# Kernel optimization log

Hardware: AMD Instinct MI355X
Metric: run time of the kernel (lower is better)

The kernel has to match this reference:

```python
import jax, jax.numpy as jnp
import numpy as np

N = 16000   # query points
M = 16000   # support points
NB = 32     # neighbors per query
A = 4       # kanchor (SO(2)/z-axis discrete anchors, kanchor<10 branch)
K = 15      # kernel points
CIN = 32
COUT = 32
RADIUS = 1.0
KP_EXTENT = 0.6


def _make_kernel_points(key):
    # KPConv-style kernel points inside a sphere of radius 0.66*RADIUS, first point at center
    kp = jax.random.normal(key, (K, 3), dtype=jnp.float32)
    kp = kp / (jnp.linalg.norm(kp, axis=-1, keepdims=True) + 1e-8)
    r = jax.random.uniform(jax.random.fold_in(key, 1), (K, 1), dtype=jnp.float32) ** (1.0 / 3.0)
    kp = kp * r * (0.66 * RADIUS)
    return kp.at[0].set(0.0)


def _make_anchors():
    # kanchor=4 -> rotations about z by 2*pi*a/A (E2PN get_anchors for kanchor<10)
    ang = 2.0 * jnp.pi * jnp.arange(A, dtype=jnp.float32) / A
    c, s = jnp.cos(ang), jnp.sin(ang)
    z = jnp.zeros_like(c)
    o = jnp.ones_like(c)
    return jnp.stack([c, -s, z, s, c, z, z, z, o], axis=-1).reshape(A, 3, 3)


def setup_inputs() -> dict:
    key = jax.random.key(0)
    k1, k2, k3, k4, k5, k6 = jax.random.split(key, 6)
    q_pts = jax.random.uniform(k1, (N, 3), dtype=jnp.float32) * 0.5
    s_pts = jax.random.uniform(k2, (M, 3), dtype=jnp.float32) * 0.5
    neighb_inds = jax.random.randint(k3, (N, NB), 0, M, dtype=jnp.int32)
    x = jax.random.normal(k4, (M, A, CIN), dtype=jnp.float32)
    kernel_points = _make_kernel_points(k5)
    anchors = _make_anchors()
    # kaiming-uniform-ish init of the (K, C_in, C_out) separable conv weights
    bound = float(np.sqrt(6.0 / ((1 + 5) * CIN)))
    weights = jax.random.uniform(k6, (K, CIN, COUT), dtype=jnp.float32,
                                 minval=-bound, maxval=bound)
    return {"q_pts": q_pts, "s_pts": s_pts, "neighb_inds": neighb_inds, "x": x,
            "kernel_points": kernel_points, "anchors": anchors, "weights": weights}


def reference(q_pts, s_pts, neighb_inds, x, kernel_points, anchors, weights):
    # neighbor gather, centered on query points: [N, NB, 3]
    neighbors = s_pts[neighb_inds] - q_pts[:, None, :]
    # rotate kernel points by each anchor: [A, K, 3]
    rot_kp = jnp.einsum('aij,kj->aki', anchors, kernel_points)
    # squared distances via |n|^2 + |kp|^2 - 2 n.kp (avoids [A,N,NB,K,3] blowup)
    n2 = jnp.sum(neighbors * neighbors, axis=-1)          # [N, NB]
    k2 = jnp.sum(rot_kp * rot_kp, axis=-1)                # [A, K]
    cross = jnp.einsum('nbj,akj->anbk', neighbors, rot_kp)
    sq_distances = n2[None, :, :, None] + k2[:, None, None, :] - 2.0 * cross  # [A,N,NB,K]
    # linear KP influence, clamped at 0
    all_weights = jnp.clip(1.0 - jnp.sqrt(jnp.maximum(sq_distances, 1e-12)) / KP_EXTENT,
                           0.0, None)                      # [A, N, NB, K]
    # gather neighbor features: [N, NB, A, C_in]
    neighb_x = x[neighb_inds]
    # weight neighbors onto kernel points (sum aggregation): [A, N, K, C_in]
    weighted_feats = jnp.einsum('anbk,nbac->ankc', all_weights, neighb_x)
    # per-kernel-point small GEMMs, summed over K: [N, A, C_out]
    out = jnp.einsum('ankc,kcd->nad', weighted_feats, weights)
    return out
```

## Files before the change

kernel.cpp:

```cpp
#include <hip/hip_runtime.h>


typedef short bf16x8 __attribute__((ext_vector_type(8)));
typedef float f32x4  __attribute__((ext_vector_type(4)));

__device__ __forceinline__ unsigned short f2bf(float f) {
    unsigned u = __builtin_bit_cast(unsigned, f);
    return (unsigned short)((u + 0x8000u) >> 16);
}

__device__ __forceinline__ unsigned pack2bf(float hi, float lo) {
    unsigned uh = __builtin_bit_cast(unsigned, hi) + 0x8000u;
    unsigned ul = __builtin_bit_cast(unsigned, lo) + 0x8000u;
    return __builtin_amdgcn_perm(uh, ul, 0x07060302u);
}

__global__ void prep_kernel(const float* __restrict__ W, unsigned short* __restrict__ Wp) {
    const int idx = blockIdx.x * 256 + threadIdx.x;
    const int kk = idx >> 10, d = (idx >> 5) & 31, e = idx & 31;
    const int kcs = kk * 32 + e;
    const int c = kcs >> 4, k = kcs & 15;
    const float v = (k < 15) ? W[(k * 32 + c) * 32 + d] : 0.0f;
    Wp[idx] = f2bf(v);
}

__global__ __launch_bounds__(256) void kpconv_mfma(
    const float* __restrict__ q_pts,
    const float* __restrict__ s_pts,
    const int*   __restrict__ inds,
    const float* __restrict__ x,
    const float* __restrict__ kp,
    const float* __restrict__ anchors,
    const unsigned short* __restrict__ Wp,
    float*       __restrict__ out)
{
    __shared__ __align__(16) unsigned short xa_s[16384];
    __shared__ __align__(16) unsigned short aw_s[8192];
    __shared__ __align__(16) float nbr[512];
    __shared__ __align__(16) float rk_s[256];
    __shared__ int sidx[128];

    const int t  = threadIdx.x;
    const int n0 = blockIdx.x * 4;

    if (t < 128) {
        const int q = t >> 5, b = t & 31;
        const int idx = inds[(n0 + q) * 32 + b];
        sidx[t] = idx;
        const float qx = q_pts[(n0 + q) * 3 + 0];
        const float qy = q_pts[(n0 + q) * 3 + 1];
        const float qz = q_pts[(n0 + q) * 3 + 2];
        const float nx = s_pts[idx * 3 + 0] - qx;
        const float ny = s_pts[idx * 3 + 1] - qy;
        const float nz = s_pts[idx * 3 + 2] - qz;
        float4 v; v.x = nx; v.y = ny; v.z = nz; v.w = nx*nx + ny*ny + nz*nz;
        *(float4*)&nbr[t * 4] = v;
    } else if (t < 192) {
        const int j = t - 128;
        const int a = j >> 4, k = j & 15;
        if (k < 15) {
            const float kx = kp[k*3+0], ky = kp[k*3+1], kz = kp[k*3+2];
            const float* R = anchors + a * 9;
            float4 v;
            v.x = R[0]*kx + R[1]*ky + R[2]*kz;
            v.y = R[3]*kx + R[4]*ky + R[5]*kz;
            v.z = R[6]*kx + R[7]*ky + R[8]*kz;
            v.w = v.x*v.x + v.y*v.y + v.z*v.z;
            *(float4*)&rk_s[(a * 16 + k) * 4] = v;
        }
    }
    __syncthreads();

    {
        const int c4 = t & 7, bg = (t >> 3) & 7, q = t >> 6;
        #pragma unroll
        for (int a = 0; a < 4; ++a) {
            float4 v[4];
            #pragma unroll
            for (int i = 0; i < 4; ++i) {
                const int row = sidx[q * 32 + 4 * bg + i];
                v[i] = ((const float4*)x)[row * 32 + a * 8 + c4];
            }
            const float* vp = (const float*)v;
            #pragma unroll
            for (int j = 0; j < 4; ++j) {
                const int c  = 4 * c4 + j;
                const int fc = c4 & 3;
                const int bb = 4 * (bg & 1) + 8 * ((bg >> 1) ^ fc);
                uint2 w;
                w.x = pack2bf(vp[1 * 4 + j], vp[0 * 4 + j]);
                w.y = pack2bf(vp[3 * 4 + j], vp[2 * 4 + j]);
                *(uint2*)&xa_s[((a * 4 + q) * 32 + c) * 32 + bb] = w;
            }
        }
    }

    {
        #pragma unroll
        for (int i = 0; i < 2; ++i) {
            const int tau = i * 256 + t;
            const int a = tau >> 7, q = (tau >> 5) & 3, b = tau & 31;
            const float4 nb = *(const float4*)&nbr[(q * 32 + b) * 4];
            unsigned short wv[16];
            #pragma unroll
            for (int k = 0; k < 15; ++k) {
                const float4 r = *(const float4*)&rk_s[(a * 16 + k) * 4];
                const float sq = nb.w + r.w - 2.0f * (nb.x*r.x + nb.y*r.y + nb.z*r.z);
                const float d = sqrtf(fmaxf(sq, 1e-12f));
                wv[k] = f2bf(fmaxf(1.0f - d * (1.0f / 0.6f), 0.0f));
            }
            wv[15] = 0;
            unsigned short* p = &aw_s[(a * 4 + q) * 512 + b];
            #pragma unroll
            for (int k = 0; k < 16; ++k) p[k * 32] = wv[k];
        }
    }
    __syncthreads();

    const int a    = t >> 6;
    const int lane = t & 63;
    const int l15  = lane & 15;
    const int quad = lane >> 4;

    unsigned short* wfb = &xa_s[a * 4096];

    #pragma unroll
    for (int q = 0; q < 4; ++q) {
        const bf16x8 afr = *(const bf16x8*)&aw_s[((a * 4 + q) * 16 + l15) * 32 + quad * 8];
        const int fc  = (l15 >> 2) & 3;
        const bf16x8 b0 = *(const bf16x8*)&xa_s[((a * 4 + q) * 32 + l15) * 32 + 8 * (quad ^ fc)];
        const bf16x8 b1 = *(const bf16x8*)&xa_s[((a * 4 + q) * 32 + l15 + 16) * 32 + 8 * (quad ^ fc)];
        f32x4 d0 = {0.f, 0.f, 0.f, 0.f}, d1 = {0.f, 0.f, 0.f, 0.f};
        d0 = __builtin_amdgcn_mfma_f32_16x16x32_bf16(afr, b0, d0, 0, 0, 0);
        d1 = __builtin_amdgcn_mfma_f32_16x16x32_bf16(afr, b1, d1, 0, 0, 0);
        uint2 s0, s1;
        s0.x = pack2bf(d0[1], d0[0]); s0.y = pack2bf(d0[3], d0[2]);
        s1.x = pack2bf(d1[1], d1[0]); s1.y = pack2bf(d1[3], d1[2]);
        *(uint2*)&wfb[q * 512 + l15 * 16 + quad * 4]        = s0;
        *(uint2*)&wfb[q * 512 + (l15 + 16) * 16 + quad * 4] = s1;
    }

    f32x4 o0 = {0.f, 0.f, 0.f, 0.f}, o1 = {0.f, 0.f, 0.f, 0.f};
    #pragma unroll
    for (int kk = 0; kk < 16; ++kk) {
        const bf16x8 a2 = *(const bf16x8*)&wfb[(l15 & 3) * 512 + kk * 32 + quad * 8];
        const bf16x8 w0 = *(const bf16x8*)&Wp[kk * 1024 + l15 * 32 + quad * 8];
        const bf16x8 w1 = *(const bf16x8*)&Wp[kk * 1024 + (l15 + 16) * 32 + quad * 8];
        o0 = __builtin_amdgcn_mfma_f32_16x16x32_bf16(a2, w0, o0, 0, 0, 0);
        o1 = __builtin_amdgcn_mfma_f32_16x16x32_bf16(a2, w1, o1, 0, 0, 0);
    }
    if (quad == 0) {
        #pragma unroll
        for (int r = 0; r < 4; ++r) {
            out[((n0 + r) * 4 + a) * 32 + l15]      = o0[r];
            out[((n0 + r) * 4 + a) * 32 + 16 + l15] = o1[r];
        }
    }
}

extern "C" void kernel_launch(void* const* d_in, const int* in_sizes, int n_in,
                              void* d_out, int out_size, void* d_ws, size_t ws_size,
                              hipStream_t stream) {
    const float* q_pts   = (const float*)d_in[0];
    const float* s_pts   = (const float*)d_in[1];
    const int*   inds    = (const int*)d_in[2];
    const float* x       = (const float*)d_in[3];
    const float* kp      = (const float*)d_in[4];
    const float* anchors = (const float*)d_in[5];
    const float* weights = (const float*)d_in[6];
    float*       out     = (float*)d_out;
    unsigned short* Wp   = (unsigned short*)d_ws;

    prep_kernel<<<dim3(64), dim3(256), 0, stream>>>(weights, Wp);
    kpconv_mfma<<<dim3(4000), dim3(256), 0, stream>>>(
        q_pts, s_pts, inds, x, kp, anchors, Wp, out);
}
```

Before: 126.7 us.

## Compute KP influence weights directly in MFMA A-fragment registers

Removes the aw_s shared buffer and its separate compute-and-scatter phase. Each lane now computes its 8 influence weights for the first MFMA's A fragment in registers, reading padded neighbor data (stride 36) and one rotated kernel point. The padded 16th kernel point gets a huge squared norm so its weight clamps to zero. The second-stage scratch writes and reads also get an XOR swizzle to reduce LDS bank conflicts. This cuts LDS traffic and footprint, which may raise occupancy, but the distance math is recomputed redundantly per lane.

```diff
diff --git a/kernel.cpp b/kernel.cpp
--- a/kernel.cpp
+++ b/kernel.cpp
@@ -35,8 +35,7 @@
     float*       __restrict__ out)
 {
     __shared__ __align__(16) unsigned short xa_s[16384];
-    __shared__ __align__(16) unsigned short aw_s[8192];
-    __shared__ __align__(16) float nbr[512];
+    __shared__ __align__(16) float nbr[576];
     __shared__ __align__(16) float rk_s[256];
     __shared__ int sidx[128];
 
@@ -54,20 +53,22 @@
         const float ny = s_pts[idx * 3 + 1] - qy;
         const float nz = s_pts[idx * 3 + 2] - qz;
         float4 v; v.x = nx; v.y = ny; v.z = nz; v.w = nx*nx + ny*ny + nz*nz;
-        *(float4*)&nbr[t * 4] = v;
+        *(float4*)&nbr[(q * 36 + b + (b >> 3)) * 4] = v;
     } else if (t < 192) {
         const int j = t - 128;
         const int a = j >> 4, k = j & 15;
+        float4 v;
         if (k < 15) {
             const float kx = kp[k*3+0], ky = kp[k*3+1], kz = kp[k*3+2];
             const float* R = anchors + a * 9;
-            float4 v;
             v.x = R[0]*kx + R[1]*ky + R[2]*kz;
             v.y = R[3]*kx + R[4]*ky + R[5]*kz;
             v.z = R[6]*kx + R[7]*ky + R[8]*kz;
             v.w = v.x*v.x + v.y*v.y + v.z*v.z;
-            *(float4*)&rk_s[(a * 16 + k) * 4] = v;
+        } else {
+            v.x = 0.0f; v.y = 0.0f; v.z = 0.0f; v.w = 1e30f;
         }
+        *(float4*)&rk_s[(a * 16 + k) * 4] = v;
     }
     __syncthreads();
 
@@ -94,58 +95,53 @@
             }
         }
     }
-
-    {
-        #pragma unroll
-        for (int i = 0; i < 2; ++i) {
-            const int tau = i * 256 + t;
-            const int a = tau >> 7, q = (tau >> 5) & 3, b = tau & 31;
-            const float4 nb = *(const float4*)&nbr[(q * 32 + b) * 4];
-            unsigned short wv[16];
-            #pragma unroll
-            for (int k = 0; k < 15; ++k) {
-                const float4 r = *(const float4*)&rk_s[(a * 16 + k) * 4];
-                const float sq = nb.w + r.w - 2.0f * (nb.x*r.x + nb.y*r.y + nb.z*r.z);
-                const float d = sqrtf(fmaxf(sq, 1e-12f));
-                wv[k] = f2bf(fmaxf(1.0f - d * (1.0f / 0.6f), 0.0f));
-            }
-            wv[15] = 0;
-            unsigned short* p = &aw_s[(a * 4 + q) * 512 + b];
-            #pragma unroll
-            for (int k = 0; k < 16; ++k) p[k * 32] = wv[k];
-        }
-    }
     __syncthreads();
 
     const int a    = t >> 6;
     const int lane = t & 63;
     const int l15  = lane & 15;
     const int quad = lane >> 4;
+    const int fc   = (l15 >> 2) & 3;
 
+    const float4 r4 = *(const float4*)&rk_s[(a * 16 + l15) * 4];
     unsigned short* wfb = &xa_s[a * 4096];
 
     #pragma unroll
     for (int q = 0; q < 4; ++q) {
-        const bf16x8 afr = *(const bf16x8*)&aw_s[((a * 4 + q) * 16 + l15) * 32 + quad * 8];
-        const int fc  = (l15 >> 2) & 3;
-        const bf16x8 b0 = *(const bf16x8*)&xa_s[((a * 4 + q) * 32 + l15) * 32 + 8 * (quad ^ fc)];
-        const bf16x8 b1 = *(const bf16x8*)&xa_s[((a * 4 + q) * 32 + l15 + 16) * 32 + 8 * (quad ^ fc)];
-        f32x4 d0 = {0.f, 0.f, 0.f, 0.f}, d1 = {0.f, 0.f, 0.f, 0.f};
+        float w8[8];
+        #pragma unroll
+        for (int j = 0; j < 8; ++j) {
+            const int b = quad * 8 + j;
+            const float4 nb = *(const float4*)&nbr[(q * 36 + b + (b >> 3)) * 4];
+            const float dot = fmaf(nb.x, r4.x, fmaf(nb.y, r4.y, nb.z * r4.z));
+            const float sq  = fmaf(-2.0f, dot, nb.w + r4.w);
+            const float d   = sqrtf(fmaxf(sq, 1e-12f));
+            w8[j] = fmaxf(fmaf(d, -(1.0f / 0.6f), 1.0f), 0.0f);
+        }
+        uint4 uu;
+        uu.x = pack2bf(w8[1], w8[0]); uu.y = pack2bf(w8[3], w8[2]);
+        uu.z = pack2bf(w8[5], w8[4]); uu.w = pack2bf(w8[7], w8[6]);
+        const bf16x8 afr = __builtin_bit_cast(bf16x8, uu);
+
+        const bf16x8 b0 = *(const bf16x8*)&xa_s[((a*4 + q)*32 + l15)      * 32 + 8 * (quad ^ fc)];
+        const bf16x8 b1 = *(const bf16x8*)&xa_s[((a*4 + q)*32 + l15 + 16) * 32 + 8 * (quad ^ fc)];
+        f32x4 d0 = {0.f,0.f,0.f,0.f}, d1 = {0.f,0.f,0.f,0.f};
         d0 = __builtin_amdgcn_mfma_f32_16x16x32_bf16(afr, b0, d0, 0, 0, 0);
         d1 = __builtin_amdgcn_mfma_f32_16x16x32_bf16(afr, b1, d1, 0, 0, 0);
         uint2 s0, s1;
         s0.x = pack2bf(d0[1], d0[0]); s0.y = pack2bf(d0[3], d0[2]);
         s1.x = pack2bf(d1[1], d1[0]); s1.y = pack2bf(d1[3], d1[2]);
-        *(uint2*)&wfb[q * 512 + l15 * 16 + quad * 4]        = s0;
-        *(uint2*)&wfb[q * 512 + (l15 + 16) * 16 + quad * 4] = s1;
+        *(uint2*)&wfb[q*512 + (( l15       * 16 + quad * 4) ^ (q * 16))] = s0;
+        *(uint2*)&wfb[q*512 + (((l15 + 16) * 16 + quad * 4) ^ (q * 16))] = s1;
     }
 
-    f32x4 o0 = {0.f, 0.f, 0.f, 0.f}, o1 = {0.f, 0.f, 0.f, 0.f};
+    const int qq = l15 & 3;
+    f32x4 o0 = {0.f,0.f,0.f,0.f}, o1 = {0.f,0.f,0.f,0.f};
     #pragma unroll
     for (int kk = 0; kk < 16; ++kk) {
-        const bf16x8 a2 = *(const bf16x8*)&wfb[(l15 & 3) * 512 + kk * 32 + quad * 8];
-        const bf16x8 w0 = *(const bf16x8*)&Wp[kk * 1024 + l15 * 32 + quad * 8];
-        const bf16x8 w1 = *(const bf16x8*)&Wp[kk * 1024 + (l15 + 16) * 32 + quad * 8];
+        const bf16x8 a2 = *(const bf16x8*)&wfb[qq*512 + ((kk*32 + quad*8) ^ (qq*16))];
+        const bf16x8 w0 = *(const bf16x8*)&Wp[kk*1024 + l15*32 + quad*8];
+        const bf16x8 w1 = *(const bf16x8*)&Wp[kk*1024 + (l15+16)*32 + quad*8];
         o0 = __builtin_amdgcn_mfma_f32_16x16x32_bf16(a2, w0, o0, 0, 0, 0);
         o1 = __builtin_amdgcn_mfma_f32_16x16x32_bf16(a2, w1, o1, 0, 0, 0);
     }
```

Result: faster. 122.7 us (-3.2%).
